# Optimization experiments

Measured on AMD Instinct MI355X. Metric: run time of the kernel, lower is better.

Reference implementation:

```python
import jax, jax.numpy as jnp
import numpy as np

DIM = 64
D_INNER = 128
D_STATE = 16
DI_M = 2 * D_INNER      # mamba expand=2
DT_RANK = 8             # ceil(d_inner/16)
DCONV = 4               # mamba default d_conv
B, T, H, W = 4, 4, 32, 16
L = T * H * W


def setup_inputs() -> dict:
    key = jax.random.key(0)
    ks = jax.random.split(key, 12)
    def s(k, shape, sc=0.02):
        return jax.random.normal(k, shape, jnp.float32) * sc
    x = jax.random.normal(ks[0], (B, T, H, W, DIM), jnp.float32)
    in_proj_w = s(ks[1], (2 * D_INNER, DIM))
    conv3d_w = s(ks[2], (D_INNER, 1, 3, 3, 3), 0.1)
    conv3d_b = jnp.zeros((D_INNER,), jnp.float32)
    out_proj_w = s(ks[3], (DIM, D_INNER))
    m_in_proj_w = s(ks[4], (2 * DI_M, D_INNER))
    m_conv1d_w = s(ks[5], (DI_M, 1, DCONV), 0.1)
    m_conv1d_b = jnp.zeros((DI_M,), jnp.float32)
    m_x_proj_w = s(ks[6], (DT_RANK + 2 * D_STATE, DI_M))
    m_dt_proj_w = s(ks[7], (DI_M, DT_RANK), 0.1)
    m_dt_proj_b = jnp.full((DI_M,), -4.6, jnp.float32)  # softplus(-4.6) ~ 0.01
    m_A_log = jnp.log(jnp.tile(jnp.arange(1, D_STATE + 1, dtype=jnp.float32), (DI_M, 1)))
    m_D = jnp.ones((DI_M,), jnp.float32)
    m_out_proj_w = s(ks[8], (D_INNER, DI_M))
    return dict(x=x, in_proj_w=in_proj_w, conv3d_w=conv3d_w, conv3d_b=conv3d_b,
                out_proj_w=out_proj_w, m_in_proj_w=m_in_proj_w, m_conv1d_w=m_conv1d_w,
                m_conv1d_b=m_conv1d_b, m_x_proj_w=m_x_proj_w, m_dt_proj_w=m_dt_proj_w,
                m_dt_proj_b=m_dt_proj_b, m_A_log=m_A_log, m_D=m_D, m_out_proj_w=m_out_proj_w)


def _silu(x):
    return x * jax.nn.sigmoid(x)


def _selective_scan(u, delta, A, Bm, Cm, Dv):
    # u, delta: [b, d, l]; A: [d, n]; Bm, Cm: [b, n, l]; Dv: [d]
    dA = jnp.exp(jnp.einsum('bdl,dn->lbdn', delta, A))          # [l,b,d,n]
    dBu = jnp.einsum('bdl,bnl,bdl->lbdn', delta, Bm, u)          # [l,b,d,n]
    C_l = jnp.transpose(Cm, (2, 0, 1))                           # [l,b,n]
    h0 = jnp.zeros(dA.shape[1:], dA.dtype)                       # [b,d,n]
    def step(h, inp):
        dA_t, dBu_t, C_t = inp
        h = dA_t * h + dBu_t
        y = jnp.einsum('bdn,bn->bd', h, C_t)
        return h, y
    _, ys = jax.lax.scan(step, h0, (dA, dBu, C_l))               # ys: [l,b,d]
    return jnp.transpose(ys, (1, 2, 0)) + Dv[None, :, None] * u  # [b,d,l]


def _mamba(xin, m_in_proj_w, m_conv1d_w, m_conv1d_b, m_x_proj_w,
           m_dt_proj_w, m_dt_proj_b, m_A_log, m_D, m_out_proj_w):
    # xin: [bb, l, d_inner]
    xz = xin @ m_in_proj_w.T                                     # [bb,l,2*di_m]
    u, z = jnp.split(xz, 2, axis=-1)
    u = jnp.transpose(u, (0, 2, 1))                              # [bb,di_m,l]
    z = jnp.transpose(z, (0, 2, 1))
    u = jax.lax.conv_general_dilated(u, m_conv1d_w, (1,), [(DCONV - 1, 0)],
                                     dimension_numbers=('NCH', 'OIH', 'NCH'),
                                     feature_group_count=DI_M) + m_conv1d_b[None, :, None]
    u = _silu(u)
    x_dbl = jnp.einsum('bdl,kd->bkl', u, m_x_proj_w)             # [bb,R+2N,l]
    dt = x_dbl[:, :DT_RANK]
    Bm = x_dbl[:, DT_RANK:DT_RANK + D_STATE]
    Cm = x_dbl[:, DT_RANK + D_STATE:]
    delta = jax.nn.softplus(jnp.einsum('dr,brl->bdl', m_dt_proj_w, dt)
                            + m_dt_proj_b[None, :, None])
    A = -jnp.exp(m_A_log)
    y = _selective_scan(u, delta, A, Bm, Cm, m_D)                # [bb,di_m,l]
    y = y * _silu(z)
    return jnp.einsum('bdl,ed->ble', y, m_out_proj_w)            # [bb,l,d_inner]


def reference(x, in_proj_w, conv3d_w, conv3d_b, out_proj_w, m_in_proj_w,
              m_conv1d_w, m_conv1d_b, m_x_proj_w, m_dt_proj_w, m_dt_proj_b,
              m_A_log, m_D, m_out_proj_w):
    xz = x @ in_proj_w.T                                         # [B,T,H,W,2*d_inner]
    xc, z = jnp.split(xz, 2, axis=-1)
    z = _silu(z)
    xc = jnp.transpose(xc, (0, 4, 1, 2, 3))                      # [B,d_inner,T,H,W]
    xc = jax.lax.conv_general_dilated(xc, conv3d_w, (1, 1, 1), [(1, 1)] * 3,
                                      dimension_numbers=('NCDHW', 'OIDHW', 'NCDHW'),
                                      feature_group_count=D_INNER)
    xc = _silu(xc + conv3d_b[None, :, None, None, None])
    seq = jnp.transpose(xc.reshape(xc.shape[0], D_INNER, L), (0, 2, 1))  # [B,L,d_inner]
    seq = jnp.concatenate([seq, seq[:, ::-1]], axis=0)           # [2B,L,d_inner]
    mixed = _mamba(seq, m_in_proj_w, m_conv1d_w, m_conv1d_b, m_x_proj_w,
                   m_dt_proj_w, m_dt_proj_b, m_A_log, m_D, m_out_proj_w)
    fwd, rev = jnp.split(mixed, 2, axis=0)
    y = (fwd + rev[:, ::-1]).reshape(x.shape[0], T, H, W, D_INNER)
    y = y * z
    return y @ out_proj_w.T
```

## Files before the change

### kernel.cpp

```cpp
#include <hip/hip_runtime.h>
#include <cmath>

#define B4   4
#define TT   4
#define HH   32
#define WW   16
#define LL   2048
#define NCH  64
#define CLEN 32
#define MEG  1048576

__device__ __forceinline__ double expd_fast(double x){
  if (x < -708.0) return 0.0;
  const double LOG2E = 1.4426950408889634074;
  const double LN2HI = 6.93147180369123816490e-01;
  const double LN2LO = 1.90821492927058770002e-10;
  double kd = rint(x*LOG2E);
  double r  = fma(-kd, LN2HI, x);
  r = fma(-kd, LN2LO, r);
  double p = 2.7557319223985888e-07;
  p = fma(p, r, 2.7557319223985890e-06);
  p = fma(p, r, 2.4801587301587302e-05);
  p = fma(p, r, 1.9841269841269841e-04);
  p = fma(p, r, 1.3888888888888889e-03);
  p = fma(p, r, 8.3333333333333333e-03);
  p = fma(p, r, 4.1666666666666664e-02);
  p = fma(p, r, 1.6666666666666666e-01);
  p = fma(p, r, 5.0e-01);
  p = fma(p, r, 1.0);
  p = fma(p, r, 1.0);
  long long ki = (long long)(1023 + (int)kd) << 52;
  return p * __longlong_as_double(ki);
}
__device__ __forceinline__ double silu_fast(double a){
  return a / (1.0 + expd_fast(-a));
}
__device__ __forceinline__ double softplus_fast(double x){
  double t = expd_fast(x);
  if (t < 0.04){
    double p = 1.0/7.0;
    p = 1.0/6.0 - t*p; p = 1.0/5.0 - t*p; p = 1.0/4.0 - t*p;
    p = 1.0/3.0 - t*p; p = 1.0/2.0 - t*p; p = 1.0 - t*p;
    return t*p;
  }
  if (x > 20.0) return x;
  return log1p(t);
}

__global__ void k_prep(const float* __restrict__ w_in, const float* __restrict__ w2,
                       const float* __restrict__ xpw, const float* __restrict__ dtw,
                       const float* __restrict__ moutw, const float* __restrict__ outw,
                       const float* __restrict__ Alog,
                       double* __restrict__ winT, double* __restrict__ w2T,
                       double* __restrict__ xpT, double* __restrict__ dtT,
                       double* __restrict__ moutT, double* __restrict__ outT,
                       double* __restrict__ ENT){
  int i = blockIdx.x*256 + threadIdx.x;
  if (i < 256*64)  winT[(i%64)*256 + i/64]   = (double)w_in[i];
  if (i < 512*128) w2T[(i%128)*512 + i/128]  = (double)w2[i];
  if (i < 40*256)  xpT[(i%256)*40 + i/256]   = (double)xpw[i];
  if (i < 256*8)   dtT[(i%8)*256 + i/8]      = (double)dtw[i];
  if (i < 128*256) moutT[(i%256)*128 + i/256]= (double)moutw[i];
  if (i < 64*128)  outT[(i%128)*64 + i/128]  = (double)outw[i];
  if (i < 16*256){ int n = i>>8, d = i&255; ENT[i] = exp((double)Alog[d*16+n]); }
}

__global__ void k_inproj(const float* __restrict__ x, const double* __restrict__ winT,
                         float* __restrict__ xc, float* __restrict__ zo){
  __shared__ float xs[64*13];
  int blk = blockIdx.x, tid = threadIdx.x;
  const float* xrow = x + (size_t)blk*8*64;
  for (int i=tid; i<8*64; i+=256){ int t=i>>6, c=i&63; xs[c*13+t] = xrow[i]; }
  __syncthreads();
  double acc[8];
  #pragma unroll
  for (int t=0;t<8;t++) acc[t]=0.0;
  for (int c=0;c<64;c++){
    double w = winT[c*256+tid];
    #pragma unroll
    for (int t=0;t<8;t++) acc[t] = fma(w, (double)xs[c*13+t], acc[t]);
  }
  int tok0 = blk*8;
  if (tid < 128){
    #pragma unroll
    for (int t=0;t<8;t++) xc[(size_t)(tok0+t)*128 + tid] = (float)acc[t];
  } else {
    int e = tid-128;
    #pragma unroll
    for (int t=0;t<8;t++) zo[(size_t)(tok0+t)*128 + e] = (float)silu_fast(acc[t]);
  }
}

__global__ void k_conv3d(const float* __restrict__ xc, const float* __restrict__ w,
                         const float* __restrict__ bias, float* __restrict__ seq){
  int blk = blockIdx.x;
  int h = blk % HH; int t = (blk/HH) % TT; int b = blk/(HH*TT);
  int c = threadIdx.x;
  double wr[27];
  #pragma unroll
  for (int i=0;i<27;i++) wr[i] = (double)w[c*27+i];
  double bv = (double)bias[c];
  const float* base = xc + (size_t)b*LL*128;
  for (int wx=0; wx<WW; wx++){
    double acc = bv;
    #pragma unroll
    for (int dt=0; dt<3; dt++){
      int tt = t+dt-1; if (tt<0||tt>TT-1) continue;
      #pragma unroll
      for (int dh=0; dh<3; dh++){
        int h2 = h+dh-1; if (h2<0||h2>HH-1) continue;
        #pragma unroll
        for (int dw=0; dw<3; dw++){
          int w2 = wx+dw-1; if (w2<0||w2>WW-1) continue;
          int l = (tt*HH+h2)*WW+w2;
          acc = fma(wr[(dt*3+dh)*3+dw], (double)base[(size_t)l*128+c], acc);
        }
      }
    }
    int l = (t*HH+h)*WW+wx;
    seq[((size_t)b*LL+l)*128+c] = (float)silu_fast(acc);
  }
}

__global__ void k_minproj(const float* __restrict__ seq, const double* __restrict__ w2T,
                          float* __restrict__ upre, float* __restrict__ zm){
  __shared__ float xs[128*13];
  int blk = blockIdx.x, tid = threadIdx.x;
  const float* srow = seq + (size_t)blk*8*128;
  for (int i=tid; i<8*128; i+=256){ int t=i>>7, c=i&127; xs[c*13+t] = srow[i]; }
  __syncthreads();
  double a0[8], a1[8];
  #pragma unroll
  for (int t=0;t<8;t++){a0[t]=0.0;a1[t]=0.0;}
  for (int c=0;c<128;c++){
    double w0 = w2T[c*512+tid];
    double w1 = w2T[c*512+tid+256];
    #pragma unroll
    for (int t=0;t<8;t++){
      double xv = (double)xs[c*13+t];
      a0[t]=fma(w0,xv,a0[t]); a1[t]=fma(w1,xv,a1[t]);
    }
  }
  int tok0=blk*8;
  #pragma unroll
  for (int t=0;t<8;t++){
    upre[(size_t)(tok0+t)*256+tid] = (float)a0[t];
    zm [(size_t)(tok0+t)*256+tid] = (float)silu_fast(a1[t]);
  }
}

__global__ void k_udelta(const float* __restrict__ upre,
                         const float* __restrict__ c1w, const float* __restrict__ c1b,
                         const double* __restrict__ xpT, const double* __restrict__ dtT,
                         const float* __restrict__ dtb,
                         float* __restrict__ U, float* __restrict__ DELTA,
                         float* __restrict__ BCb){
  __shared__ float us[16*256];
  __shared__ double xdbl[16*40];
  int tile = blockIdx.x, db = blockIdx.y;
  int dir = db>>2, b = db&3;
  int d = threadIdx.x;
  double w0=(double)c1w[d*4+0], w1=(double)c1w[d*4+1], w2=(double)c1w[d*4+2], w3=(double)c1w[d*4+3];
  double cbv=(double)c1b[d];
  double dtbv=(double)dtb[d];
  double dtw[8];
  #pragma unroll
  for (int r=0;r<8;r++) dtw[r] = dtT[r*256+d];
  int l0 = tile*16;
  auto src = [&](int l)->double{
    if (l < 0) return 0.0;
    int lo = dir ? (LL-1-l) : l;
    return (double)upre[((size_t)b*LL+lo)*256+d];
  };
  double x0=src(l0-3), x1=src(l0-2), x2=src(l0-1);
  for (int i=0;i<16;i++){
    double x3 = src(l0+i);
    double a = cbv + w0*x0 + w1*x1 + w2*x2 + w3*x3;
    float uv = (float)silu_fast(a);
    us[i*256+d] = uv;
    U[((size_t)db*LL + l0+i)*256 + d] = uv;
    x0=x1; x1=x2; x2=x3;
  }
  __syncthreads();
  {
    int j = d & 63, grp = d >> 6;
    if (j < 40){
      double acc[4]={0.0,0.0,0.0,0.0};
      for (int c=0;c<256;c++){
        double wv = xpT[c*40+j];
        #pragma unroll
        for (int i2=0;i2<4;i2++) acc[i2] = fma(wv, (double)us[(grp*4+i2)*256+c], acc[i2]);
      }
      #pragma unroll
      for (int i2=0;i2<4;i2++) xdbl[(grp*4+i2)*40+j] = acc[i2];
    }
  }
  __syncthreads();
  for (int t=0;t<16;t++){
    double dacc = dtbv;
    #pragma unroll
    for (int r=0;r<8;r++) dacc = fma(dtw[r], xdbl[t*40+r], dacc);
    double delta = softplus_fast(dacc);
    DELTA[((size_t)db*LL + l0+t)*256 + d] = (float)delta;
  }
  for (int i=d; i<512; i+=256){
    int t = i>>5, n = i&31;
    BCb[((size_t)db*LL + l0+t)*32 + n] = (float)xdbl[t*40+8+n];
  }
}

template<int PASS>
__global__ void k_scanP(const float* __restrict__ U, const float* __restrict__ DELTA,
                        const float* __restrict__ BCb, const double* __restrict__ ENT,
                        const float* __restrict__ Dv, const float* __restrict__ zm,
                        const float* __restrict__ hin,
                        float* __restrict__ S, float* __restrict__ SD,
                        float* __restrict__ yf){
  int ch = blockIdx.x, db = blockIdx.y;
  int dir = db>>2, b = db&3;
  int d = threadIdx.x;
  double cn[16];
  #pragma unroll
  for (int n=0;n<16;n++) cn[n] = ENT[n*256+d] - (double)(n+1);
  double h[16];
  if (PASS==0){
    #pragma unroll
    for (int n=0;n<16;n++) h[n]=0.0;
  } else {
    #pragma unroll
    for (int n=0;n<16;n++) h[n] = (double)hin[(((size_t)db*NCH+ch)*16+n)*256+d];
  }
  double Dd = (double)Dv[d];
  double Sd = 0.0;
  int l0 = ch*CLEN;
  const float* dp = DELTA + ((size_t)db*LL + l0)*256 + d;
  const float* up = U     + ((size_t)db*LL + l0)*256 + d;
  const float* bp = BCb   + ((size_t)db*LL + l0)*32;
  #pragma unroll 4
  for (int i=0;i<CLEN;i++){
    double dl = (double)dp[(size_t)i*256];
    double uv = (double)up[(size_t)i*256];
    if (PASS==0) Sd += dl;
    double e1 = expd_fast(-dl);
    double du = dl*uv;
    double e2 = e1*e1, e4 = e2*e2, e8 = e4*e4;
    double p1=e1,      p2=e2,      p3=e2*e1,   p4=e4;
    double p5=p1*e4,   p6=p2*e4,   p7=p3*e4,   p8=e8;
    double p9=p1*e8,   p10=p2*e8,  p11=p3*e8,  p12=p4*e8;
    double p13=p5*e8,  p14=p6*e8,  p15=p7*e8,  p16=p8*e8;
    double y = 0.0;
    #define SCAN_STEP(n, pw) { \
      double dA = (pw) * fma(-dl, cn[n], 1.0); \
      h[n] = fma(dA, h[n], du*(double)bp[i*32+(n)]); \
      if (PASS==1) y = fma(h[n], (double)bp[i*32+16+(n)], y); }
    SCAN_STEP(0,p1)  SCAN_STEP(1,p2)  SCAN_STEP(2,p3)  SCAN_STEP(3,p4)
    SCAN_STEP(4,p5)  SCAN_STEP(5,p6)  SCAN_STEP(6,p7)  SCAN_STEP(7,p8)
    SCAN_STEP(8,p9)  SCAN_STEP(9,p10) SCAN_STEP(10,p11) SCAN_STEP(11,p12)
    SCAN_STEP(12,p13) SCAN_STEP(13,p14) SCAN_STEP(14,p15) SCAN_STEP(15,p16)
    #undef SCAN_STEP
    if (PASS==1){
      int l = l0 + i;
      y = fma(Dd, uv, y);
      int lo = dir ? (LL-1-l) : l;
      y *= (double)zm[((size_t)b*LL+lo)*256+d];
      yf[((size_t)db*LL+l)*256+d] = (float)y;
    }
  }
  if (PASS==0){
    #pragma unroll
    for (int n=0;n<16;n++) S[(((size_t)db*NCH+ch)*16+n)*256+d] = (float)h[n];
    SD[((size_t)db*NCH+ch)*256+d] = (float)Sd;
  }
}

__global__ void k_scanB(const float* __restrict__ S, const float* __restrict__ SD,
                        const double* __restrict__ ENT, float* __restrict__ hin){
  int n = blockIdx.x, db = blockIdx.y;
  int d = threadIdx.x;
  double en = ENT[n*256+d];
  double h = 0.0;
  for (int ch=0; ch<NCH; ch++){
    size_t idx = (((size_t)db*NCH+ch)*16+n)*256+d;
    hin[idx] = (float)h;
    double Sd = (double)SD[((size_t)db*NCH+ch)*256+d];
    h = fma(expd_fast(-Sd*en), h, (double)S[idx]);
  }
}

__global__ void k_out(const float* __restrict__ yf, const double* __restrict__ moutT,
                      const float* __restrict__ zo, const double* __restrict__ outT,
                      float* __restrict__ out){
  __shared__ float cs[256*13];
  __shared__ float ys[128*13];
  int blk = blockIdx.x, tid = threadIdx.x;
  int tok0 = blk*8;
  int b = tok0 / LL; int l0 = tok0 % LL;
  for (int i=tid; i<8*256; i+=256){
    int t = i>>8, d = i&255;
    int l = l0+t;
    cs[d*13+t] = yf[((size_t)b*LL + l)*256 + d] + yf[((size_t)(4+b)*LL + (LL-1-l))*256 + d];
  }
  __syncthreads();
  int e = tid & 127; int gh = tid >> 7;
  double acc[4];
  #pragma unroll
  for (int i=0;i<4;i++) acc[i]=0.0;
  for (int d=0; d<256; d++){
    double wv = moutT[d*128+e];
    #pragma unroll
    for (int i=0;i<4;i++) acc[i] = fma(wv, (double)cs[d*13+gh*4+i], acc[i]);
  }
  #pragma unroll
  for (int i=0;i<4;i++){
    int t = gh*4+i;
    double zv = (double)zo[(size_t)(tok0+t)*128 + e];
    ys[e*13+t] = (float)(acc[i]*zv);
  }
  __syncthreads();
  int o = tid & 63; int g4 = tid>>6;
  double acc2[2];
  #pragma unroll
  for (int i=0;i<2;i++) acc2[i]=0.0;
  for (int ee=0; ee<128; ee++){
    double wv = outT[ee*64+o];
    #pragma unroll
    for (int i=0;i<2;i++) acc2[i] = fma(wv, (double)ys[ee*13+g4*2+i], acc2[i]);
  }
  #pragma unroll
  for (int i=0;i<2;i++) out[(size_t)(tok0 + g4*2+i)*64 + o] = (float)acc2[i];
}

extern "C" void kernel_launch(void* const* d_in, const int* in_sizes, int n_in,
                              void* d_out, int out_size, void* d_ws, size_t ws_size,
                              hipStream_t stream){
  const float* x     = (const float*)d_in[0];
  const float* w_in  = (const float*)d_in[1];
  const float* c3w   = (const float*)d_in[2];
  const float* c3b   = (const float*)d_in[3];
  const float* outw  = (const float*)d_in[4];
  const float* w2    = (const float*)d_in[5];
  const float* c1w   = (const float*)d_in[6];
  const float* c1b   = (const float*)d_in[7];
  const float* xpw   = (const float*)d_in[8];
  const float* dtw   = (const float*)d_in[9];
  const float* dtb   = (const float*)d_in[10];
  const float* Alog  = (const float*)d_in[11];
  const float* Dv    = (const float*)d_in[12];
  const float* moutw = (const float*)d_in[13];
  float* ws = (float*)d_ws;
  float* UPRE = ws + 0;
  float* HIN  = UPRE;
  float* ZM   = ws + 2*MEG;
  float* U    = ws + 4*MEG;
  float* XC   = ws + 4*MEG;
  float* DELTA= ws + 8*MEG;
  float* SEQ  = ws + 8*MEG;
  float* BCb  = ws + 12*MEG;
  float* ZO   = ws + 12*MEG + 524288;
  float* YF   = ws + 13*MEG + 524288;
  float* Sb   = YF;
  float* SDb  = ws + 17*MEG + 524288;
  double* WT  = (double*)(ws + 17*MEG + 524288 + 131072);
  double* winT  = WT;
  double* w2T   = winT + 16384;
  double* xpT   = w2T + 65536;
  double* dtT   = xpT + 10240;
  double* moutT = dtT + 2048;
  double* outT  = moutT + 32768;
  double* ENT   = outT + 8192;
  float* out = (float*)d_out;

  k_prep   <<<dim3(256),     dim3(256), 0, stream>>>(w_in, w2, xpw, dtw, moutw, outw, Alog,
                                                     winT, w2T, xpT, dtT, moutT, outT, ENT);
  k_inproj <<<dim3(1024),    dim3(256), 0, stream>>>(x, winT, XC, ZO);
  k_conv3d <<<dim3(512),     dim3(128), 0, stream>>>(XC, c3w, c3b, SEQ);
  k_minproj<<<dim3(1024),    dim3(256), 0, stream>>>(SEQ, w2T, UPRE, ZM);
  k_udelta <<<dim3(128,8),   dim3(256), 0, stream>>>(UPRE, c1w, c1b, xpT, dtT, dtb,
                                                     U, DELTA, BCb);
  k_scanP<0><<<dim3(NCH,8),  dim3(256), 0, stream>>>(U, DELTA, BCb, ENT, Dv, ZM,
                                                     nullptr, Sb, SDb, nullptr);
  k_scanB  <<<dim3(16,8),    dim3(256), 0, stream>>>(Sb, SDb, ENT, HIN);
  k_scanP<1><<<dim3(NCH,8),  dim3(256), 0, stream>>>(U, DELTA, BCb, ENT, Dv, ZM,
                                                     HIN, nullptr, nullptr, YF);
  k_out    <<<dim3(1024),    dim3(256), 0, stream>>>(YF, moutT, ZO, outT, out);
}
```

Baseline: 389.3 us.

## Double scan chunks, merge directions via atomicAdd, in-place carry propagation

Halves chunk length and doubles the number of scan chunks so the fp64 scan kernels launch more blocks. The forward and reverse directions now atomically add into a shared combined buffer, so the output kernel reads one value per token instead of summing two. The carry kernel writes its prefix states in place over the chunk-state buffer. The power chain is also computed by serial multiplication. The cost is a memset, float atomics with nondeterministic summation order, and a longer serial loop in k_scanB.

```diff
diff --git a/kernel.cpp b/kernel.cpp
--- a/kernel.cpp
+++ b/kernel.cpp
@@ -6,8 +6,8 @@
 #define HH   32
 #define WW   16
 #define LL   2048
-#define NCH  64
-#define CLEN 32
+#define NCH  128
+#define CLEN 16
 #define MEG  1048576
 
 __device__ __forceinline__ double expd_fast(double x){
@@ -215,7 +215,7 @@
                         const float* __restrict__ Dv, const float* __restrict__ zm,
                         const float* __restrict__ hin,
                         float* __restrict__ S, float* __restrict__ SD,
-                        float* __restrict__ yf){
+                        float* __restrict__ yc){
   int ch = blockIdx.x, db = blockIdx.y;
   int dir = db>>2, b = db&3;
   int d = threadIdx.x;
@@ -243,27 +243,21 @@
     if (PASS==0) Sd += dl;
     double e1 = expd_fast(-dl);
     double du = dl*uv;
-    double e2 = e1*e1, e4 = e2*e2, e8 = e4*e4;
-    double p1=e1,      p2=e2,      p3=e2*e1,   p4=e4;
-    double p5=p1*e4,   p6=p2*e4,   p7=p3*e4,   p8=e8;
-    double p9=p1*e8,   p10=p2*e8,  p11=p3*e8,  p12=p4*e8;
-    double p13=p5*e8,  p14=p6*e8,  p15=p7*e8,  p16=p8*e8;
+    double pw = 1.0;
     double y = 0.0;
-    #define SCAN_STEP(n, pw) { \
-      double dA = (pw) * fma(-dl, cn[n], 1.0); \
-      h[n] = fma(dA, h[n], du*(double)bp[i*32+(n)]); \
-      if (PASS==1) y = fma(h[n], (double)bp[i*32+16+(n)], y); }
-    SCAN_STEP(0,p1)  SCAN_STEP(1,p2)  SCAN_STEP(2,p3)  SCAN_STEP(3,p4)
-    SCAN_STEP(4,p5)  SCAN_STEP(5,p6)  SCAN_STEP(6,p7)  SCAN_STEP(7,p8)
-    SCAN_STEP(8,p9)  SCAN_STEP(9,p10) SCAN_STEP(10,p11) SCAN_STEP(11,p12)
-    SCAN_STEP(12,p13) SCAN_STEP(13,p14) SCAN_STEP(14,p15) SCAN_STEP(15,p16)
-    #undef SCAN_STEP
+    #pragma unroll
+    for (int n=0;n<16;n++){
+      pw *= e1;
+      double dA = pw * fma(-dl, cn[n], 1.0);
+      h[n] = fma(dA, h[n], du*(double)bp[i*32+n]);
+      if (PASS==1) y = fma(h[n], (double)bp[i*32+16+n], y);
+    }
     if (PASS==1){
       int l = l0 + i;
       y = fma(Dd, uv, y);
       int lo = dir ? (LL-1-l) : l;
       y *= (double)zm[((size_t)b*LL+lo)*256+d];
-      yf[((size_t)db*LL+l)*256+d] = (float)y;
+      atomicAdd(&yc[((size_t)b*LL+lo)*256+d], (float)y);
     }
   }
   if (PASS==0){
@@ -273,32 +267,31 @@
   }
 }
 
-__global__ void k_scanB(const float* __restrict__ S, const float* __restrict__ SD,
-                        const double* __restrict__ ENT, float* __restrict__ hin){
+__global__ void k_scanB(float* __restrict__ S, const float* __restrict__ SD,
+                        const double* __restrict__ ENT){
   int n = blockIdx.x, db = blockIdx.y;
   int d = threadIdx.x;
   double en = ENT[n*256+d];
   double h = 0.0;
   for (int ch=0; ch<NCH; ch++){
     size_t idx = (((size_t)db*NCH+ch)*16+n)*256+d;
-    hin[idx] = (float)h;
+    double Sl = (double)S[idx];
+    S[idx] = (float)h;
     double Sd = (double)SD[((size_t)db*NCH+ch)*256+d];
-    h = fma(expd_fast(-Sd*en), h, (double)S[idx]);
-  }
-}
-
-__global__ void k_out(const float* __restrict__ yf, const double* __restrict__ moutT,
+    h = fma(expd_fast(-Sd*en), h, Sl);
+  }
+}
+
+__global__ void k_out(const float* __restrict__ yc, const double* __restrict__ moutT,
                       const float* __restrict__ zo, const double* __restrict__ outT,
                       float* __restrict__ out){
   __shared__ float cs[256*13];
   __shared__ float ys[128*13];
   int blk = blockIdx.x, tid = threadIdx.x;
   int tok0 = blk*8;
-  int b = tok0 / LL; int l0 = tok0 % LL;
   for (int i=tid; i<8*256; i+=256){
     int t = i>>8, d = i&255;
-    int l = l0+t;
-    cs[d*13+t] = yf[((size_t)b*LL + l)*256 + d] + yf[((size_t)(4+b)*LL + (LL-1-l))*256 + d];
+    cs[d*13+t] = yc[(size_t)(tok0+t)*256 + d];
   }
   __syncthreads();
   int e = tid & 127; int gh = tid >> 7;
@@ -349,7 +342,6 @@
   const float* moutw = (const float*)d_in[13];
   float* ws = (float*)d_ws;
   float* UPRE = ws + 0;
-  float* HIN  = UPRE;
   float* ZM   = ws + 2*MEG;
   float* U    = ws + 4*MEG;
   float* XC   = ws + 4*MEG;
@@ -357,10 +349,10 @@
   float* SEQ  = ws + 8*MEG;
   float* BCb  = ws + 12*MEG;
   float* ZO   = ws + 12*MEG + 524288;
-  float* YF   = ws + 13*MEG + 524288;
-  float* Sb   = YF;
-  float* SDb  = ws + 17*MEG + 524288;
-  double* WT  = (double*)(ws + 17*MEG + 524288 + 131072);
+  float* YC   = ws + 13*MEG + 524288;
+  float* Sb   = ws + 15*MEG + 524288;
+  float* SDb  = ws + 19*MEG + 524288;
+  double* WT  = (double*)(ws + 19*MEG + 524288 + 262144);
   double* winT  = WT;
   double* w2T   = winT + 16384;
   double* xpT   = w2T + 65536;
@@ -372,6 +364,7 @@
 
   k_prep   <<<dim3(256),     dim3(256), 0, stream>>>(w_in, w2, xpw, dtw, moutw, outw, Alog,
                                                      winT, w2T, xpT, dtT, moutT, outT, ENT);
+  hipMemsetAsync(YC, 0, 2*MEG*sizeof(float), stream);
   k_inproj <<<dim3(1024),    dim3(256), 0, stream>>>(x, winT, XC, ZO);
   k_conv3d <<<dim3(512),     dim3(128), 0, stream>>>(XC, c3w, c3b, SEQ);
   k_minproj<<<dim3(1024),    dim3(256), 0, stream>>>(SEQ, w2T, UPRE, ZM);
@@ -379,8 +372,8 @@
                                                      U, DELTA, BCb);
   k_scanP<0><<<dim3(NCH,8),  dim3(256), 0, stream>>>(U, DELTA, BCb, ENT, Dv, ZM,
                                                      nullptr, Sb, SDb, nullptr);
-  k_scanB  <<<dim3(16,8),    dim3(256), 0, stream>>>(Sb, SDb, ENT, HIN);
+  k_scanB  <<<dim3(16,8),    dim3(256), 0, stream>>>(Sb, SDb, ENT);
   k_scanP<1><<<dim3(NCH,8),  dim3(256), 0, stream>>>(U, DELTA, BCb, ENT, Dv, ZM,
-                                                     HIN, nullptr, nullptr, YF);
-  k_out    <<<dim3(1024),    dim3(256), 0, stream>>>(YF, moutT, ZO, outT, out);
-}
+                                                     Sb, nullptr, nullptr, YC);
+  k_out    <<<dim3(1024),    dim3(256), 0, stream>>>(YC, moutT, ZO, outT, out);
+}
```

After: 363.9 us. 6.5% less time.
